# Kernel tuning notes

Hardware: AMD Instinct MI355X
Metric: run time of the kernel (lower is better)

The kernel has to match this reference:

```python
import jax, jax.numpy as jnp
import numpy as np

B, S, H = 8, 4096, 1024
N_GATHER = 65536
NUM_SEGMENTS = 16384


def setup_inputs() -> dict:
    key = jax.random.key(0)
    ks = jax.random.split(key, 7)
    transformer_hidden = jax.random.normal(ks[0], (B, S, H), dtype=jnp.float32)
    dense_w = jax.random.normal(ks[1], (H, H), dtype=jnp.float32) * (1.0 / np.sqrt(H))
    dense_b = jax.random.normal(ks[2], (H,), dtype=jnp.float32) * 0.02
    proj_w = jax.random.normal(ks[3], (H,), dtype=jnp.float32) * (1.0 / np.sqrt(H))
    proj_b = jax.random.normal(ks[4], (1,), dtype=jnp.float32) * 0.02
    flat_indices = jax.random.randint(ks[5], (N_GATHER,), 0, B * S, dtype=jnp.int32)
    segment_ids = jnp.sort(jax.random.randint(ks[6], (N_GATHER,), 0, NUM_SEGMENTS, dtype=jnp.int32))
    return {
        "transformer_hidden": transformer_hidden,
        "dense_w": dense_w,
        "dense_b": dense_b,
        "proj_w": proj_w,
        "proj_b": proj_b,
        "flat_indices": flat_indices,
        "segment_ids": segment_ids,
    }


def reference(transformer_hidden, dense_w, dense_b, proj_w, proj_b, flat_indices, segment_ids):
    # Flatten [B,S,H] -> [B*S,H] and gather per-object token hidden states.
    flat = transformer_hidden.reshape(-1, H)
    gathered = flat[flat_indices]  # [N_GATHER, H]
    # Ragged per-group mean (variable-length index sets).
    sums = jax.ops.segment_sum(gathered, segment_ids, num_segments=NUM_SEGMENTS)  # [G, H]
    counts = jax.ops.segment_sum(
        jnp.ones((N_GATHER,), dtype=gathered.dtype), segment_ids, num_segments=NUM_SEGMENTS
    )
    h = sums / jnp.maximum(counts, 1.0)[:, None]  # [G, H]
    # dense -> gelu -> linear head (torch F.gelu is exact, not tanh approx)
    z = jax.nn.gelu(h @ dense_w.T + dense_b, approximate=False)
    predictions = z @ proj_w + proj_b  # [G]
    return predictions.reshape(-1)
```

## Files before the change

kernel.cpp:

```cpp
#include <hip/hip_runtime.h>

#define H 1024
#define NROWS 32768
#define NG 65536
#define NSEG 16384

#define BM 128
#define BN 128
#define BK 64

typedef __attribute__((ext_vector_type(8))) short bf16x8;
typedef __attribute__((ext_vector_type(4))) float f32x4;

__device__ __forceinline__ unsigned short f2bf(float x) {
    unsigned u = __builtin_bit_cast(unsigned, x);
    unsigned r = (u + 0x7fffu + ((u >> 16) & 1u)) >> 16;
    return (unsigned short)r;
}

__device__ __forceinline__ void gload_lds16(const void* g, void* l) {
    __builtin_amdgcn_global_load_lds(
        (const __attribute__((address_space(1))) void*)g,
        (__attribute__((address_space(3))) void*)l, 16, 0, 0);
}

__global__ void seg_bounds_kernel(const int* __restrict__ seg, int* __restrict__ seg_start) {
    int g = blockIdx.x * 256 + threadIdx.x;
    if (g > NSEG) return;
    if (g == NSEG) { seg_start[g] = NG; return; }
    int lo = 0, hi = NG;
    while (lo < hi) { int mid = (lo + hi) >> 1; if (seg[mid] < g) lo = mid + 1; else hi = mid; }
    seg_start[g] = lo;
}

__global__ void convert_w_kernel(const float* __restrict__ w, unsigned short* __restrict__ wbf) {
    int i = (blockIdx.x * 256 + threadIdx.x) * 4;
    float4 v = *(const float4*)(w + i);
    ushort4 o;
    o.x = f2bf(v.x); o.y = f2bf(v.y); o.z = f2bf(v.z); o.w = f2bf(v.w);
    *(ushort4*)(wbf + i) = o;
}

__global__ void init_out_kernel(float* __restrict__ out, const float* __restrict__ proj_b) {
    int i = blockIdx.x * 256 + threadIdx.x;
    if (i < NSEG) out[i] = proj_b[0];
}

__global__ void seg_mean_kernel(const float* __restrict__ hidden,
                                const int* __restrict__ flat_indices,
                                const int* __restrict__ seg_start,
                                unsigned short* __restrict__ hbf) {
    int g = blockIdx.x;
    int t = threadIdx.x;
    int s = seg_start[g], e = seg_start[g + 1];
    float4 acc = {0.f, 0.f, 0.f, 0.f};
    for (int i = s; i < e; ++i) {
        int row = flat_indices[i];
        float4 v = *((const float4*)(hidden + (size_t)row * H) + t);
        acc.x += v.x; acc.y += v.y; acc.z += v.z; acc.w += v.w;
    }
    float scale = (e > s) ? 1.0f / (float)(e - s) : 0.0f;
    ushort4 o;
    o.x = f2bf(acc.x * scale); o.y = f2bf(acc.y * scale);
    o.z = f2bf(acc.z * scale); o.w = f2bf(acc.w * scale);
    *(ushort4*)(hbf + (size_t)g * H + t * 4) = o;
}

__global__ __launch_bounds__(256, 2) void gemm_kernel(
    const unsigned short* __restrict__ Abf,
    const unsigned short* __restrict__ Wbf,
    const float* __restrict__ dense_b,
    const float* __restrict__ proj_w,
    float* __restrict__ out) {
    __shared__ unsigned short As[BM * BK];
    __shared__ unsigned short Bs[BN * BK];
    const int tid = threadIdx.x;
    const int wid = tid >> 6, lane = tid & 63;
    const int wr = wid >> 1, wc = wid & 1;
    const int m0 = blockIdx.x * BM, n0 = blockIdx.y * BN;

    f32x4 acc[4][4] = {};

    for (int kt = 0; kt < H / BK; ++kt) {
#pragma unroll
        for (int it = 0; it < 4; ++it) {
            int c = it * 256 + tid;
            int row = c >> 3;
            int sw = ((c & 7) << 4) ^ ((row & 7) << 4);
            gload_lds16((const char*)Abf + (((size_t)(m0 + row)) << 11) + kt * 128 + sw,
                        (char*)As + (it * 256 + wid * 64) * 16);
            gload_lds16((const char*)Wbf + (((size_t)(n0 + row)) << 11) + kt * 128 + sw,
                        (char*)Bs + (it * 256 + wid * 64) * 16);
        }
        __syncthreads();
#pragma unroll
        for (int kk = 0; kk < 2; ++kk) {
            bf16x8 af[4], bfr[4];
            int kb = kk * 64 + ((lane >> 4) << 4);
#pragma unroll
            for (int mi = 0; mi < 4; ++mi) {
                int row = wr * 64 + mi * 16 + (lane & 15);
                af[mi] = *(const bf16x8*)((const char*)As + row * 128 + (kb ^ ((row & 7) << 4)));
            }
#pragma unroll
            for (int ni = 0; ni < 4; ++ni) {
                int row = wc * 64 + ni * 16 + (lane & 15);
                bfr[ni] = *(const bf16x8*)((const char*)Bs + row * 128 + (kb ^ ((row & 7) << 4)));
            }
#pragma unroll
            for (int mi = 0; mi < 4; ++mi)
#pragma unroll
                for (int ni = 0; ni < 4; ++ni)
                    acc[mi][ni] = __builtin_amdgcn_mfma_f32_16x16x32_bf16(af[mi], bfr[ni], acc[mi][ni], 0, 0, 0);
        }
        __syncthreads();
    }

#pragma unroll
    for (int mi = 0; mi < 4; ++mi) {
#pragma unroll
        for (int r = 0; r < 4; ++r) {
            int m = m0 + wr * 64 + mi * 16 + ((lane >> 4) << 2) + r;
            float s = 0.f;
#pragma unroll
            for (int ni = 0; ni < 4; ++ni) {
                int n = n0 + wc * 64 + ni * 16 + (lane & 15);
                float z = acc[mi][ni][r] + dense_b[n];
                float gl = 0.5f * z * (1.0f + erff(z * 0.70710678118f));
                s += gl * proj_w[n];
            }
#pragma unroll
            for (int off = 1; off < 16; off <<= 1) s += __shfl_xor(s, off, 64);
            if ((lane & 15) == 0) atomicAdd(out + m, s);
        }
    }
}

extern "C" void kernel_launch(void* const* d_in, const int* in_sizes, int n_in,
                              void* d_out, int out_size, void* d_ws, size_t ws_size,
                              hipStream_t stream) {
    const float* hidden       = (const float*)d_in[0];
    const float* dense_w      = (const float*)d_in[1];
    const float* dense_b      = (const float*)d_in[2];
    const float* proj_w       = (const float*)d_in[3];
    const float* proj_b       = (const float*)d_in[4];
    const int*   flat_indices = (const int*)d_in[5];
    const int*   segment_ids  = (const int*)d_in[6];
    float* out = (float*)d_out;

    char* ws = (char*)d_ws;
    int* seg_start = (int*)ws;
    unsigned short* hbf = (unsigned short*)(ws + (1 << 17));
    unsigned short* wbf = (unsigned short*)(ws + (1 << 17) + (size_t)NSEG * H * 2);

    hipLaunchKernelGGL(seg_bounds_kernel, dim3(65), dim3(256), 0, stream, segment_ids, seg_start);
    hipLaunchKernelGGL(convert_w_kernel, dim3(H * H / 1024), dim3(256), 0, stream, dense_w, wbf);
    hipLaunchKernelGGL(init_out_kernel, dim3(64), dim3(256), 0, stream, out, proj_b);
    hipLaunchKernelGGL(seg_mean_kernel, dim3(NSEG), dim3(256), 0, stream, hidden, flat_indices, seg_start, hbf);
    hipLaunchKernelGGL(gemm_kernel, dim3(NSEG / BM, H / BN), dim3(256), 0, stream, hbf, wbf, dense_b, proj_w, out);
}
```

Before: 103.4 us.

## Double-buffer GEMM with 256x256 tiles and merge setup kernels into one launch

The GEMM tile grows to 256x256 with 512 threads, and the K loop is double-buffered: the next LDS stage is loaded while the current one is computed, using explicit vmcnt waits, barriers and a raised wave priority around the MFMA block. The epilogue loads bias and projection weights into registers once. The three small setup kernels (weight conversion, output init, segment bounds) are merged into one launch to cut launch overhead. The GEMM grid drops to 256 blocks, which may underfill the GPU, and the larger tiles and accumulators raise register and LDS pressure, which can limit occupancy.

```diff
diff --git a/kernel.cpp b/kernel.cpp
--- a/kernel.cpp
+++ b/kernel.cpp
@@ -1,13 +1,13 @@
 #include <hip/hip_runtime.h>
 
 #define H 1024
-#define NROWS 32768
 #define NG 65536
 #define NSEG 16384
 
-#define BM 128
-#define BN 128
+#define BM 256
+#define BN 256
 #define BK 64
+#define NT (H / BK)
 
 typedef __attribute__((ext_vector_type(8))) short bf16x8;
 typedef __attribute__((ext_vector_type(4))) float f32x4;
@@ -24,26 +24,29 @@
         (__attribute__((address_space(3))) void*)l, 16, 0, 0);
 }
 
-__global__ void seg_bounds_kernel(const int* __restrict__ seg, int* __restrict__ seg_start) {
-    int g = blockIdx.x * 256 + threadIdx.x;
-    if (g > NSEG) return;
-    if (g == NSEG) { seg_start[g] = NG; return; }
-    int lo = 0, hi = NG;
-    while (lo < hi) { int mid = (lo + hi) >> 1; if (seg[mid] < g) lo = mid + 1; else hi = mid; }
-    seg_start[g] = lo;
-}
+#define CFENCE() asm volatile("" ::: "memory")
 
-__global__ void convert_w_kernel(const float* __restrict__ w, unsigned short* __restrict__ wbf) {
-    int i = (blockIdx.x * 256 + threadIdx.x) * 4;
-    float4 v = *(const float4*)(w + i);
-    ushort4 o;
-    o.x = f2bf(v.x); o.y = f2bf(v.y); o.z = f2bf(v.z); o.w = f2bf(v.w);
-    *(ushort4*)(wbf + i) = o;
-}
-
-__global__ void init_out_kernel(float* __restrict__ out, const float* __restrict__ proj_b) {
-    int i = blockIdx.x * 256 + threadIdx.x;
-    if (i < NSEG) out[i] = proj_b[0];
+__global__ void setup_kernel(const float* __restrict__ w, unsigned short* __restrict__ wbf,
+                             const float* __restrict__ proj_b, float* __restrict__ out,
+                             const int* __restrict__ seg, int* __restrict__ seg_start) {
+    int b = blockIdx.x;
+    if (b < 1024) {
+        int i = (b * 256 + threadIdx.x) * 4;
+        float4 v = *(const float4*)(w + i);
+        ushort4 o;
+        o.x = f2bf(v.x); o.y = f2bf(v.y); o.z = f2bf(v.z); o.w = f2bf(v.w);
+        *(ushort4*)(wbf + i) = o;
+    } else if (b < 1088) {
+        int i = (b - 1024) * 256 + threadIdx.x;
+        if (i < NSEG) out[i] = proj_b[0];
+    } else {
+        int g = (b - 1088) * 256 + threadIdx.x;
+        if (g > NSEG) return;
+        if (g == NSEG) { seg_start[g] = NG; return; }
+        int lo = 0, hi = NG;
+        while (lo < hi) { int mid = (lo + hi) >> 1; if (seg[mid] < g) lo = mid + 1; else hi = mid; }
+        seg_start[g] = lo;
+    }
 }
 
 __global__ void seg_mean_kernel(const float* __restrict__ hidden,
@@ -66,68 +69,99 @@
     *(ushort4*)(hbf + (size_t)g * H + t * 4) = o;
 }
 
-__global__ __launch_bounds__(256, 2) void gemm_kernel(
+__global__ __launch_bounds__(512, 2) void gemm_kernel(
     const unsigned short* __restrict__ Abf,
     const unsigned short* __restrict__ Wbf,
     const float* __restrict__ dense_b,
     const float* __restrict__ proj_w,
     float* __restrict__ out) {
-    __shared__ unsigned short As[BM * BK];
-    __shared__ unsigned short Bs[BN * BK];
+    __shared__ unsigned short As[2][BM * BK];
+    __shared__ unsigned short Bs[2][BN * BK];
     const int tid = threadIdx.x;
     const int wid = tid >> 6, lane = tid & 63;
-    const int wr = wid >> 1, wc = wid & 1;
+    const int wr = wid >> 2, wc = wid & 3;
     const int m0 = blockIdx.x * BM, n0 = blockIdx.y * BN;
 
-    f32x4 acc[4][4] = {};
+    f32x4 acc[8][4] = {};
 
-    for (int kt = 0; kt < H / BK; ++kt) {
+    auto STAGE = [&](int buf, int kt) {
 #pragma unroll
         for (int it = 0; it < 4; ++it) {
-            int c = it * 256 + tid;
+            int c = it * 512 + tid;
             int row = c >> 3;
             int sw = ((c & 7) << 4) ^ ((row & 7) << 4);
             gload_lds16((const char*)Abf + (((size_t)(m0 + row)) << 11) + kt * 128 + sw,
-                        (char*)As + (it * 256 + wid * 64) * 16);
+                        (char*)&As[buf][0] + (it * 512 + wid * 64) * 16);
+        }
+#pragma unroll
+        for (int it = 0; it < 4; ++it) {
+            int c = it * 512 + tid;
+            int row = c >> 3;
+            int sw = ((c & 7) << 4) ^ ((row & 7) << 4);
             gload_lds16((const char*)Wbf + (((size_t)(n0 + row)) << 11) + kt * 128 + sw,
-                        (char*)Bs + (it * 256 + wid * 64) * 16);
+                        (char*)&Bs[buf][0] + (it * 512 + wid * 64) * 16);
         }
-        __syncthreads();
+    };
+
+    STAGE(0, 0);
+
+    for (int t = 0; t < NT; ++t) {
+        CFENCE();
+        __builtin_amdgcn_s_barrier();
+        CFENCE();
+        if (t + 1 < NT) {
+            STAGE((t + 1) & 1, t + 1);
+            asm volatile("s_waitcnt vmcnt(8)" ::: "memory");
+        } else {
+            asm volatile("s_waitcnt vmcnt(0)" ::: "memory");
+        }
+        __builtin_amdgcn_s_barrier();
+        CFENCE();
+
+        const char* Ab = (const char*)&As[t & 1][0];
+        const char* Bb = (const char*)&Bs[t & 1][0];
+        __builtin_amdgcn_s_setprio(1);
 #pragma unroll
         for (int kk = 0; kk < 2; ++kk) {
-            bf16x8 af[4], bfr[4];
+            bf16x8 af[8], bw[4];
             int kb = kk * 64 + ((lane >> 4) << 4);
-#pragma unroll
-            for (int mi = 0; mi < 4; ++mi) {
-                int row = wr * 64 + mi * 16 + (lane & 15);
-                af[mi] = *(const bf16x8*)((const char*)As + row * 128 + (kb ^ ((row & 7) << 4)));
-            }
 #pragma unroll
             for (int ni = 0; ni < 4; ++ni) {
                 int row = wc * 64 + ni * 16 + (lane & 15);
-                bfr[ni] = *(const bf16x8*)((const char*)Bs + row * 128 + (kb ^ ((row & 7) << 4)));
+                bw[ni] = *(const bf16x8*)(Bb + row * 128 + (kb ^ ((row & 7) << 4)));
             }
 #pragma unroll
-            for (int mi = 0; mi < 4; ++mi)
+            for (int mi = 0; mi < 8; ++mi) {
+                int row = wr * 128 + mi * 16 + (lane & 15);
+                af[mi] = *(const bf16x8*)(Ab + row * 128 + (kb ^ ((row & 7) << 4)));
+            }
+#pragma unroll
+            for (int mi = 0; mi < 8; ++mi)
 #pragma unroll
                 for (int ni = 0; ni < 4; ++ni)
-                    acc[mi][ni] = __builtin_amdgcn_mfma_f32_16x16x32_bf16(af[mi], bfr[ni], acc[mi][ni], 0, 0, 0);
+                    acc[mi][ni] = __builtin_amdgcn_mfma_f32_16x16x32_bf16(af[mi], bw[ni], acc[mi][ni], 0, 0, 0);
         }
-        __syncthreads();
+        __builtin_amdgcn_s_setprio(0);
     }
 
+    float db[4], pw[4];
 #pragma unroll
-    for (int mi = 0; mi < 4; ++mi) {
+    for (int ni = 0; ni < 4; ++ni) {
+        int n = n0 + wc * 64 + ni * 16 + (lane & 15);
+        db[ni] = dense_b[n];
+        pw[ni] = proj_w[n];
+    }
+#pragma unroll
+    for (int mi = 0; mi < 8; ++mi) {
 #pragma unroll
         for (int r = 0; r < 4; ++r) {
-            int m = m0 + wr * 64 + mi * 16 + ((lane >> 4) << 2) + r;
+            int m = m0 + wr * 128 + mi * 16 + ((lane >> 4) << 2) + r;
             float s = 0.f;
 #pragma unroll
             for (int ni = 0; ni < 4; ++ni) {
-                int n = n0 + wc * 64 + ni * 16 + (lane & 15);
-                float z = acc[mi][ni][r] + dense_b[n];
+                float z = acc[mi][ni][r] + db[ni];
                 float gl = 0.5f * z * (1.0f + erff(z * 0.70710678118f));
-                s += gl * proj_w[n];
+                s += gl * pw[ni];
             }
 #pragma unroll
             for (int off = 1; off < 16; off <<= 1) s += __shfl_xor(s, off, 64);
@@ -153,9 +187,10 @@
     unsigned short* hbf = (unsigned short*)(ws + (1 << 17));
     unsigned short* wbf = (unsigned short*)(ws + (1 << 17) + (size_t)NSEG * H * 2);
 
-    hipLaunchKernelGGL(seg_bounds_kernel, dim3(65), dim3(256), 0, stream, segment_ids, seg_start);
-    hipLaunchKernelGGL(convert_w_kernel, dim3(H * H / 1024), dim3(256), 0, stream, dense_w, wbf);
-    hipLaunchKernelGGL(init_out_kernel, dim3(64), dim3(256), 0, stream, out, proj_b);
-    hipLaunchKernelGGL(seg_mean_kernel, dim3(NSEG), dim3(256), 0, stream, hidden, flat_indices, seg_start, hbf);
-    hipLaunchKernelGGL(gemm_kernel, dim3(NSEG / BM, H / BN), dim3(256), 0, stream, hbf, wbf, dense_b, proj_w, out);
+    hipLaunchKernelGGL(setup_kernel, dim3(1153), dim3(256), 0, stream,
+                       dense_w, wbf, proj_b, out, segment_ids, seg_start);
+    hipLaunchKernelGGL(seg_mean_kernel, dim3(NSEG), dim3(256), 0, stream,
+                       hidden, flat_indices, seg_start, hbf);
+    hipLaunchKernelGGL(gemm_kernel, dim3(NSEG / BM, H / BN), dim3(512), 0, stream,
+                       hbf, wbf, dense_b, proj_w, out);
 }
```

Result: no change. 103.5 us, median of 2 (+0.1%).
